# Optimization experiments

Measured on AMD Instinct MI355X. Metric: run time of the kernel, lower is better.

Reference implementation:

```python
import jax, jax.numpy as jnp
import numpy as np
from jax import lax

B, T = 4, 2048
IN_CH, SKIP_CH, OUT_CH, K = 256, 128, 128, 5
N_MAMBA, D_STATE, D_CONV, EXPAND = 2, 16, 4, 2
D_INNER = EXPAND * OUT_CH
DT_RANK = (OUT_CH + 15) // 16  # ceil(d_model/16) = 8
L = 2 * T
EPS = 1e-5


def setup_inputs() -> dict:
    key = jax.random.key(0)
    ks = jax.random.split(key, 16)
    def rn(k, shape, s=0.02):
        return jax.random.normal(k, shape, jnp.float32) * s
    A_init = jnp.broadcast_to(jnp.arange(1, D_STATE + 1, dtype=jnp.float32),
                              (N_MAMBA, 2, D_INNER, D_STATE))
    return {
        'x': rn(ks[0], (B, IN_CH, T), 1.0),
        'skip': rn(ks[1], (B, SKIP_CH, L), 1.0),
        'up_w': rn(ks[2], (IN_CH, IN_CH, K)),       # torch ConvTranspose1d weight (in,out,k)
        'up_b': jnp.zeros((IN_CH,), jnp.float32),
        'fus_w': rn(ks[3], (OUT_CH, IN_CH + SKIP_CH)),  # 1x1 conv
        'fus_b': jnp.zeros((OUT_CH,), jnp.float32),
        'gn_w': jnp.ones((OUT_CH,), jnp.float32),
        'gn_b': jnp.zeros((OUT_CH,), jnp.float32),
        'prelu_a': jnp.array(0.25, jnp.float32),
        'ln_w': jnp.ones((N_MAMBA, OUT_CH), jnp.float32),
        'ln_b': jnp.zeros((N_MAMBA, OUT_CH), jnp.float32),
        'in_w': rn(ks[4], (N_MAMBA, 2, 2 * D_INNER, OUT_CH)),
        'conv_w': rn(ks[5], (N_MAMBA, 2, D_INNER, D_CONV), 0.1),
        'conv_b': jnp.zeros((N_MAMBA, 2, D_INNER), jnp.float32),
        'xproj_w': rn(ks[6], (N_MAMBA, 2, DT_RANK + 2 * D_STATE, D_INNER)),
        'dtproj_w': rn(ks[7], (N_MAMBA, 2, D_INNER, DT_RANK), 0.1),
        'dtproj_b': rn(ks[8], (N_MAMBA, 2, D_INNER), 0.1),
        'A_log': jnp.log(A_init),
        'Dp': jnp.ones((N_MAMBA, 2, D_INNER), jnp.float32),
        'out_w': rn(ks[9], (N_MAMBA, 2, OUT_CH, D_INNER)),
    }


def _mamba_branch(xn, cw, cb, iw, xw, dw, db, Alog, Dp, ow):
    # xn: [B, L, d_model] -> [B, L, d_model]; standard Mamba selective scan.
    xz = jnp.einsum('bld,ed->ble', xn, iw)            # [B,L,2*D_INNER]
    xi, z = jnp.split(xz, 2, axis=-1)
    # causal depthwise conv over time
    xc = lax.conv_general_dilated(xi.transpose(0, 2, 1), cw[:, None, :], (1,),
                                  [(D_CONV - 1, 0)], feature_group_count=D_INNER,
                                  dimension_numbers=('NCH', 'OIH', 'NCH'))
    xi = jax.nn.silu(xc + cb[None, :, None]).transpose(0, 2, 1)  # [B,L,D_INNER]
    dbl = jnp.einsum('bld,ed->ble', xi, xw)           # [B,L,DT_RANK+2N]
    dt = jax.nn.softplus(jnp.einsum('blr,dr->bld', dbl[..., :DT_RANK], dw) + db)
    Bc = dbl[..., DT_RANK:DT_RANK + D_STATE]          # [B,L,N]
    Cc = dbl[..., DT_RANK + D_STATE:]                 # [B,L,N]
    A = -jnp.exp(Alog)                                # [D_INNER,N]
    dA = jnp.exp(dt[..., None] * A)                   # [B,L,D_INNER,N]
    dBx = dt[..., None] * Bc[:, :, None, :] * xi[..., None]
    def comb(c1, c2):
        a1, b1 = c1
        a2, b2 = c2
        return a1 * a2, a2 * b1 + b2
    _, h = lax.associative_scan(comb, (dA, dBx), axis=1)  # h_t = dA_t h_{t-1} + dBx_t
    y = jnp.einsum('bldn,bln->bld', h, Cc) + Dp * xi
    return jnp.einsum('ble,de->bld', y * jax.nn.silu(z), ow)


def _forward(x, skip, up_w, up_b, fus_w, fus_b, gn_w, gn_b, prelu_a, ln_w, ln_b,
             in_w, conv_w, conv_b, xproj_w, dtproj_w, dtproj_b, A_log, Dp, out_w):
    p = K // 2
    # ConvTranspose1d(stride=2, padding=p, output_padding=1) == lhs-dilated conv with flipped kernel
    wt = jnp.flip(up_w, -1).transpose(1, 0, 2)        # (out,in,k)
    u = lax.conv_general_dilated(x, wt, (1,), [(K - 1 - p, K - 1 - p + 1)],
                                 lhs_dilation=(2,),
                                 dimension_numbers=('NCH', 'OIH', 'NCH'))
    u = u + up_b[None, :, None]
    u = u[..., :skip.shape[-1]]
    h = jnp.concatenate([u, skip], axis=1)            # [B, in+skip, L]
    h = jnp.einsum('bct,oc->bot', h, fus_w) + fus_b[None, :, None]
    # GroupNorm(1, C): normalize over (C,T) per sample
    mu = h.mean(axis=(1, 2), keepdims=True)
    var = h.var(axis=(1, 2), keepdims=True)
    h = (h - mu) / jnp.sqrt(var + EPS) * gn_w[None, :, None] + gn_b[None, :, None]
    h = jnp.where(h >= 0, h, prelu_a * h)             # PReLU (single param)
    h = h.transpose(0, 2, 1)                          # [B, L, C]
    for i in range(N_MAMBA):
        # BiMambaBlock: pre-LN, forward + time-reversed Mamba, residual sum
        mu2 = h.mean(-1, keepdims=True)
        v2 = h.var(-1, keepdims=True)
        xn = (h - mu2) / jnp.sqrt(v2 + EPS) * ln_w[i] + ln_b[i]
        f = _mamba_branch(xn, conv_w[i, 0], conv_b[i, 0], in_w[i, 0], xproj_w[i, 0],
                          dtproj_w[i, 0], dtproj_b[i, 0], A_log[i, 0], Dp[i, 0], out_w[i, 0])
        b = _mamba_branch(jnp.flip(xn, 1), conv_w[i, 1], conv_b[i, 1], in_w[i, 1], xproj_w[i, 1],
                          dtproj_w[i, 1], dtproj_b[i, 1], A_log[i, 1], Dp[i, 1], out_w[i, 1])
        h = h + f + jnp.flip(b, 1)
    return h.transpose(0, 2, 1)                       # [B, C_out, L]


def reference(x, skip, up_w, up_b, fus_w, fus_b, gn_w, gn_b, prelu_a, ln_w, ln_b,
              in_w, conv_w, conv_b, xproj_w, dtproj_w, dtproj_b, A_log, Dp, out_w):
    return _forward(x, skip, up_w, up_b, fus_w, fus_b, gn_w, gn_b, prelu_a, ln_w, ln_b,
                    in_w, conv_w, conv_b, xproj_w, dtproj_w, dtproj_b, A_log, Dp, out_w)
```

## Files before the change

kernel.cpp:

```cpp
#include <hip/hip_runtime.h>
#include <hip/hip_bf16.h>

#define Bsz 4
#define Tt 2048
#define Ll 4096
#define NC 256
#define CH 16

typedef short bf16x8 __attribute__((ext_vector_type(8)));
typedef float f32x4 __attribute__((ext_vector_type(4)));
typedef float f32x2 __attribute__((ext_vector_type(2)));

static __device__ __forceinline__ f32x2 pk_fma(f32x2 a, f32x2 b, f32x2 c){
  f32x2 d;
  asm("v_pk_fma_f32 %0, %1, %2, %3" : "=v"(d) : "v"(a), "v"(b), "v"(c));
  return d;
}
static __device__ __forceinline__ f32x2 pk_mul(f32x2 a, f32x2 b){
  f32x2 d;
  asm("v_pk_mul_f32 %0, %1, %2" : "=v"(d) : "v"(a), "v"(b));
  return d;
}
static __device__ __forceinline__ f32x2 lo2(f32x4 v){ return (f32x2){v.x, v.y}; }
static __device__ __forceinline__ f32x2 hi2(f32x4 v){ return (f32x2){v.z, v.w}; }

static __device__ __forceinline__ float bs2f(unsigned short u){
  union{float f; unsigned int i;} v; v.i = ((unsigned int)u)<<16; return v.f;
}
static __device__ __forceinline__ unsigned short f2bs(float f){
  union{float f; unsigned int i;} v; v.f = f;
  unsigned int r = (v.i + 0x7fffu + ((v.i>>16)&1u)) >> 16;
  return (unsigned short)r;
}

__global__ void k_cvt(const float* __restrict__ src, unsigned short* __restrict__ dst, int n){
  int i = blockIdx.x*256 + threadIdx.x;
  if (i < n) dst[i] = f2bs(src[i]);
}

__global__ void k_prepx(const float* __restrict__ xw, unsigned short* __restrict__ wxb){
  int row = blockIdx.x, br = blockIdx.y, col = threadIdx.x;
  float v = (row < 40) ? xw[((size_t)br*40 + row)*256 + col] : 0.f;
  wxb[((size_t)br*64 + row)*256 + col] = f2bs(v);
}

__global__ void k_prepA(const float* __restrict__ Alog, float* __restrict__ AEX,
                        float* __restrict__ A0C, float* __restrict__ CHN){
  int br = blockIdx.x, d = threadIdx.x;
  float A[16];
  #pragma unroll
  for (int j=0;j<4;j++){
    float4 a4 = *(const float4*)&Alog[(size_t)br*4096 + d*16 + j*4];
    A[4*j]  = -__expf(a4.x); A[4*j+1] = -__expf(a4.y);
    A[4*j+2]= -__expf(a4.z); A[4*j+3] = -__expf(a4.w);
    *(float4*)&AEX[(size_t)br*4096 + d*16 + j*4] = (float4){A[4*j],A[4*j+1],A[4*j+2],A[4*j+3]};
  }
  bool chain = true;
  #pragma unroll
  for (int n=1;n<16;n++){
    float expect = A[0]*(float)(n+1);
    if (fabsf(A[n]-expect) > 1e-3f*fabsf(expect)) chain = false;
  }
  A0C[br*256 + d] = A[0];
  CHN[br*256 + d] = chain ? 1.f : 0.f;
}

__global__ void k_compose(const float* __restrict__ up_w, const float* __restrict__ fus_w,
                          const float* __restrict__ fus_b, const float* __restrict__ up_b,
                          unsigned short* __restrict__ WEb, unsigned short* __restrict__ WOb,
                          unsigned short* __restrict__ FWSb, float* __restrict__ BIAS2){
  int i = blockIdx.x;
  int o = threadIdx.x;
  float a0=0.f,a1=0.f,a2=0.f,a3=0.f,a4=0.f;
  for (int c=0;c<256;c++){
    float f = fus_w[o*384+c];
    const float* w = up_w + ((size_t)i*256+c)*5;
    a0 += f*w[0]; a1 += f*w[1]; a2 += f*w[2];
    a3 += f*w[3]; a4 += f*w[4];
  }
  WEb[(size_t)o*768 +       i] = f2bs(a4);
  WEb[(size_t)o*768 + 256 + i] = f2bs(a2);
  WEb[(size_t)o*768 + 512 + i] = f2bs(a0);
  WOb[(size_t)o*512 +       i] = f2bs(a3);
  WOb[(size_t)o*512 + 256 + i] = f2bs(a1);
  if (i<128) FWSb[o*128 + i] = f2bs(fus_w[o*384+256+i]);
  if (i==0){
    float bb = fus_b[o];
    for (int c=0;c<256;c++) bb += fus_w[o*384+c]*up_b[c];
    BIAS2[o]=bb;
  }
// ... 368 lines not shown
  int tid = threadIdx.x;
  int dir = blockIdx.y;
  xz  += (size_t)dir*Bsz*Ll*512;
  wxb += (size_t)dir*64*256;
  cw  += dir*1024;
  cb  += dir*256;
  xib += (size_t)dir*Bsz*Ll*256;
  dbl += (size_t)dir*Bsz*Ll*40;
  size_t row0 = (size_t)blockIdx.x*64;
  int p0 = (int)(row0 & (Ll-1));

  {
    int d = tid;
    float4 w4 = *(const float4*)&cw[d*4];
    float bias = cb[d];
    float w0, w1, w2;
    if (p0 == 0){ w0=0.f; w1=0.f; w2=0.f; }
    else {
      w0 = bs2f(xz[(row0-3)*512 + d]);
      w1 = bs2f(xz[(row0-2)*512 + d]);
      w2 = bs2f(xz[(row0-1)*512 + d]);
    }
    #pragma unroll 4
    for (int rr=0; rr<64; rr++){
      float xv = bs2f(xz[(row0+rr)*512 + d]);
      float acc = bias + w4.x*w0 + w4.y*w1 + w4.z*w2 + w4.w*xv;
      float v = acc*__builtin_amdgcn_rcpf(1.f+__expf(-acc));
      unsigned short us = f2bs(v);
      xiS[rr*264 + d] = us;
      xib[(row0+rr)*256 + d] = us;
      w0=w1; w1=w2; w2=xv;
    }
  }

  int wave = tid>>6, lane = tid&63;
  int quad = lane>>4, l16 = lane&15;
  f32x4 acc[4];
  #pragma unroll
  for (int j=0;j<4;j++) acc[j] = (f32x4){0.f,0.f,0.f,0.f};

  for (int kb=0; kb<256; kb+=64){
    __syncthreads();
    #pragma unroll
    for (int it=0; it<2; it++){
      int idx = it*256 + tid;
      int row = idx>>3, c8 = idx&7;
      *(uint4*)&Bs[row*72 + c8*8] = *(const uint4*)&wxb[(size_t)row*256 + kb + c8*8];
    }
    __syncthreads();
    #pragma unroll
    for (int ks=0; ks<64; ks+=32){
      bf16x8 af = *(bf16x8*)&xiS[(wave*16+l16)*264 + kb + ks + quad*8];
      #pragma unroll
      for (int nt=0;nt<4;nt++){
        bf16x8 bf = *(bf16x8*)&Bs[(nt*16+l16)*72 + ks + quad*8];
        acc[nt] = __builtin_amdgcn_mfma_f32_16x16x32_bf16(af, bf, acc[nt], 0,0,0);
      }
    }
  }
  #pragma unroll
  for (int nt=0;nt<4;nt++)
    #pragma unroll
    for (int r=0;r<4;r++){
      int m = wave*16 + quad*4 + r;
      int col = nt*16 + l16;
      if (col < 40) dbl[(row0+m)*40 + col] = acc[nt][r];
    }
}

#define POWTREE2(e1, pw2) { \
  float _e2 = (e1)*(e1); \
  f32x2 _e2v = (f32x2){_e2,_e2}; \
  pw2[0] = (f32x2){(e1),_e2}; \
  pw2[1] = pk_mul(pw2[0], _e2v); \
  pw2[2] = pk_mul(pw2[1], _e2v); \
  pw2[3] = pk_mul(pw2[2], _e2v); \
  f32x2 _e8v = (f32x2){pw2[3].y, pw2[3].y}; \
  pw2[4] = pk_mul(pw2[0], _e8v); \
  pw2[5] = pk_mul(pw2[1], _e8v); \
  pw2[6] = pk_mul(pw2[2], _e8v); \
  pw2[7] = pk_mul(pw2[3], _e8v); }

__global__ __launch_bounds__(256) void k_scan1(const float* __restrict__ dbl,
                       const unsigned short* __restrict__ xib, const float* __restrict__ AEX,
                       const float* __restrict__ A0C, const float* __restrict__ CHNf,
                       const float* __restrict__ dtw, const float* __restrict__ dtb,
                       float* __restrict__ SD, float* __restrict__ Q){
  __shared__ float dblS[CH*24];
  int b = blockIdx.y, c = blockIdx.x, dir = blockIdx.z;
  int d = threadIdx.x;
  const float* dblP = dbl + (size_t)dir*Bsz*Ll*40;
  const unsigned short* xiP = xib + (size_t)dir*Bsz*Ll*256;
  size_t base = (size_t)b*Ll + (size_t)c*CH;
  if (d < CH*6){
    int p = d/6, j = d - p*6;
    *(float4*)&dblS[p*24 + j*4] = *(const float4*)&dblP[(base+p)*40 + j*4];
  }
  float A0 = A0C[dir*256 + d];
  bool chain = CHNf[dir*256 + d] != 0.f;
  f32x2 wv2[4];
  {
    const float* dw = dtw + (size_t)dir*2048 + d*8;
    float4 w0 = *(const float4*)&dw[0];
    float4 w1 = *(const float4*)&dw[4];
    wv2[0]=(f32x2){w0.x,w0.y}; wv2[1]=(f32x2){w0.z,w0.w};
    wv2[2]=(f32x2){w1.x,w1.y}; wv2[3]=(f32x2){w1.z,w1.w};
  }
  float bbt = dtb[dir*256 + d];
  __syncthreads();
  float sdt = 0.f;
  const unsigned short* xip = xiP + base*256 + d;
  size_t sbase = (size_t)dir*Bsz*NC*4096 + ((size_t)(b*NC + c))*4096 + (size_t)d*16;
  if (chain){
    bool n1 = fabsf(A0 + 1.f) < 1e-6f;
    float xv[CH];
    #pragma unroll
    for (int p=0;p<CH;p++) xv[p] = bs2f(xip[(size_t)p*256]);
    f32x2 h2[8];
    #pragma unroll
    for (int i=0;i<8;i++) h2[i] = (f32x2){0.f,0.f};
    #pragma unroll
    for (int p=0;p<CH;p++){
      const float* rw = &dblS[p*24];
      f32x4 t0 = *(const f32x4*)&rw[0];
      f32x4 t1 = *(const f32x4*)&rw[4];
      f32x2 dp = pk_mul(lo2(t0), wv2[0]);
      dp = pk_fma(hi2(t0), wv2[1], dp);
      dp = pk_fma(lo2(t1), wv2[2], dp);
      dp = pk_fma(hi2(t1), wv2[3], dp);
      float a0 = bbt + dp.x + dp.y;
      float t = __expf(a0);
      float u = 1.f + t;
      float dtv = (a0>20.f)? a0 : __logf(u);
      float e1 = n1 ? __builtin_amdgcn_rcpf(u) : __expf(dtv*A0);
      float dx = dtv*xv[p];
      sdt += dtv;
      f32x2 pw2[8];
      POWTREE2(e1, pw2);
      f32x2 dxv = (f32x2){dx,dx};
      f32x4 b0 = *(const f32x4*)&dblS[p*24+8];
      f32x4 b1 = *(const f32x4*)&dblS[p*24+12];
      f32x4 b2 = *(const f32x4*)&dblS[p*24+16];
      f32x4 b3 = *(const f32x4*)&dblS[p*24+20];
      h2[0] = pk_fma(pw2[0], h2[0], pk_mul(lo2(b0), dxv));
      h2[1] = pk_fma(pw2[1], h2[1], pk_mul(hi2(b0), dxv));
      h2[2] = pk_fma(pw2[2], h2[2], pk_mul(lo2(b1), dxv));
      h2[3] = pk_fma(pw2[3], h2[3], pk_mul(hi2(b1), dxv));
      h2[4] = pk_fma(pw2[4], h2[4], pk_mul(lo2(b2), dxv));
      h2[5] = pk_fma(pw2[5], h2[5], pk_mul(hi2(b2), dxv));
      h2[6] = pk_fma(pw2[6], h2[6], pk_mul(lo2(b3), dxv));
      h2[7] = pk_fma(pw2[7], h2[7], pk_mul(hi2(b3), dxv));
    }
    #pragma unroll
    for (int j=0;j<4;j++)
      *(float4*)&Q[sbase + 4*j] = (float4){h2[2*j].x,h2[2*j].y,h2[2*j+1].x,h2[2*j+1].y};
  } else {
    float A[16];
    #pragma unroll
    for (int j=0;j<4;j++)
      *(float4*)&A[4*j] = *(const float4*)&AEX[(size_t)dir*4096 + d*16 + j*4];
    float h[16];
    #pragma unroll
    for (int n=0;n<16;n++) h[n]=0.f;
    for (int p=0;p<CH;p++){
      const float* rw = &dblS[p*24];
      float4 t0 = *(const float4*)&rw[0], t1 = *(const float4*)&rw[4];
      float a0 = bbt + t0.x*wv2[0].x+t0.y*wv2[0].y+t0.z*wv2[1].x+t0.w*wv2[1].y
                     + t1.x*wv2[2].x+t1.y*wv2[2].y+t1.z*wv2[3].x+t1.w*wv2[3].y;
      float dtv = (a0>20.f)? a0 : __logf(1.f+__expf(a0));
      float xiv = bs2f(xip[(size_t)p*256]);
      float dx = dtv*xiv;
      sdt += dtv;
      float bc[16];
      *(float4*)&bc[0]  = *(const float4*)&rw[8];
      *(float4*)&bc[4]  = *(const float4*)&rw[12];
      *(float4*)&bc[8]  = *(const float4*)&rw[16];
      *(float4*)&bc[12] = *(const float4*)&rw[20];
      #pragma unroll
      for (int n=0;n<16;n++){
        float a = __expf(dtv*A[n]);
        h[n] = a*h[n] + bc[n]*dx;
      }
    }
    #pragma unroll
    for (int j=0;j<4;j++)
      *(float4*)&Q[sbase + 4*j] = (float4){h[4*j],h[4*j+1],h[4*j+2],h[4*j+3]};
  }
  SD[(((size_t)dir*Bsz + b)*NC + c)*256 + d] = sdt;
}

__global__ __launch_bounds__(64) void k_scan2(const float* __restrict__ SD, float* __restrict__ Q,
                                              const float* __restrict__ AEX){
  int b = blockIdx.y, dir = blockIdx.z;
  int t = blockIdx.x*64 + threadIdx.x;
  int dn4 = t*4;
  int d = dn4 >> 4;
  float4 A4 = *(const float4*)&AEX[(size_t)dir*4096 + dn4];
  const float* sd = SD + (((size_t)dir*Bsz + b)*NC)*256 + d;
  float* q = Q + (size_t)dir*Bsz*NC*4096 + (size_t)b*NC*4096 + dn4;
  float4 H = {0.f,0.f,0.f,0.f};
  float  s_n = sd[0];
  float4 q_n = *(const float4*)q;
  for (int c=0;c<NC;c++){
    float s_c = s_n; float4 q_c = q_n;
    if (c+1 < NC){
      s_n = sd[(size_t)(c+1)*256];
      q_n = *(const float4*)(q + (size_t)(c+1)*4096);
    }
    float4 p;
    p.x = __expf(A4.x*s_c); p.y = __expf(A4.y*s_c);
    p.z = __expf(A4.z*s_c); p.w = __expf(A4.w*s_c);
    *(float4*)(q + (size_t)c*4096) = H;
    H.x = p.x*H.x + q_c.x; H.y = p.y*H.y + q_c.y;
    H.z = p.z*H.z + q_c.z; H.w = p.w*H.w + q_c.w;
  }
}

__global__ __launch_bounds__(256) void k_scan3(const float* __restrict__ dbl,
                       unsigned short* xiy, const float* __restrict__ AEX,
                       const float* __restrict__ A0C, const float* __restrict__ CHNf,
                       const float* __restrict__ dtw, const float* __restrict__ dtb,
                       const float* __restrict__ Dpw, const float* __restrict__ Hs,
                       const unsigned short* __restrict__ xz){
  __shared__ float dblS[CH*40];
  int b = blockIdx.y, c = blockIdx.x, dir = blockIdx.z;
  int d = threadIdx.x;
  const float* dblP = dbl + (size_t)dir*Bsz*Ll*40;
  unsigned short* xiP = xiy + (size_t)dir*Bsz*Ll*256;
  const unsigned short* xzP = xz + (size_t)dir*Bsz*Ll*512;
  size_t base = (size_t)b*Ll + (size_t)c*CH;
  for (int idx=d; idx<CH*10; idx+=256){
    int p = idx/10, j = idx - p*10;
    *(float4*)&dblS[p*40 + j*4] = *(const float4*)&dblP[(base+p)*40 + j*4];
  }
  float A0 = A0C[dir*256 + d];
  bool chain = CHNf[dir*256 + d] != 0.f;
  f32x2 wv2[4];
  {
    const float* dw = dtw + (size_t)dir*2048 + d*8;
    float4 w0 = *(const float4*)&dw[0];
    float4 w1 = *(const float4*)&dw[4];
    wv2[0]=(f32x2){w0.x,w0.y}; wv2[1]=(f32x2){w0.z,w0.w};
    wv2[2]=(f32x2){w1.x,w1.y}; wv2[3]=(f32x2){w1.z,w1.w};
  }
  float bbt = dtb[dir*256 + d];
  float Dp = Dpw[dir*256 + d];
  size_t sbase = (size_t)dir*Bsz*NC*4096 + ((size_t)(b*NC + c))*4096 + (size_t)d*16;
  __syncthreads();
  unsigned short* xip = xiP + base*256 + d;
  const unsigned short* zp = xzP + base*512 + 256 + d;
  if (chain){
    bool n1 = fabsf(A0 + 1.f) < 1e-6f;
    float xv[CH], zv[CH];
    #pragma unroll
    for (int p=0;p<CH;p++) xv[p] = bs2f(xip[(size_t)p*256]);
    #pragma unroll
    for (int p=0;p<CH;p++) zv[p] = bs2f(zp[(size_t)p*512]);
    f32x2 h2[8];
    #pragma unroll
    for (int j=0;j<4;j++){
      float4 h4 = *(const float4*)&Hs[sbase + 4*j];
      h2[2*j]   = (f32x2){h4.x,h4.y};
      h2[2*j+1] = (f32x2){h4.z,h4.w};
    }
    #pragma unroll
    for (int p=0;p<CH;p++){
      const float* rw = &dblS[p*40];
      f32x4 t0 = *(const f32x4*)&rw[0];
      f32x4 t1 = *(const f32x4*)&rw[4];
      f32x2 dp = pk_mul(lo2(t0), wv2[0]);
      dp = pk_fma(hi2(t0), wv2[1], dp);
      dp = pk_fma(lo2(t1), wv2[2], dp);
      dp = pk_fma(hi2(t1), wv2[3], dp);
      float a0 = bbt + dp.x + dp.y;
      float t = __expf(a0);
      float u = 1.f + t;
      float dtv = (a0>20.f)? a0 : __logf(u);
      float e1 = n1 ? __builtin_amdgcn_rcpf(u) : __expf(dtv*A0);
      float dx = dtv*xv[p];
      f32x2 pw2[8];
      POWTREE2(e1, pw2);
      f32x2 dxv = (f32x2){dx,dx};
      f32x4 b0 = *(const f32x4*)&dblS[p*40+8];
      f32x4 b1 = *(const f32x4*)&dblS[p*40+12];
      f32x4 b2 = *(const f32x4*)&dblS[p*40+16];
      f32x4 b3 = *(const f32x4*)&dblS[p*40+20];
      f32x4 c0 = *(const f32x4*)&dblS[p*40+24];
      f32x4 c1 = *(const f32x4*)&dblS[p*40+28];
      f32x4 c2 = *(const f32x4*)&dblS[p*40+32];
      f32x4 c3 = *(const f32x4*)&dblS[p*40+36];
      f32x2 ya;
      h2[0] = pk_fma(pw2[0], h2[0], pk_mul(lo2(b0), dxv));
      ya = pk_mul(h2[0], lo2(c0));
      h2[1] = pk_fma(pw2[1], h2[1], pk_mul(hi2(b0), dxv));
      ya = pk_fma(h2[1], hi2(c0), ya);
      h2[2] = pk_fma(pw2[2], h2[2], pk_mul(lo2(b1), dxv));
      ya = pk_fma(h2[2], lo2(c1), ya);
      h2[3] = pk_fma(pw2[3], h2[3], pk_mul(hi2(b1), dxv));
      ya = pk_fma(h2[3], hi2(c1), ya);
      h2[4] = pk_fma(pw2[4], h2[4], pk_mul(lo2(b2), dxv));
      ya = pk_fma(h2[4], lo2(c2), ya);
      h2[5] = pk_fma(pw2[5], h2[5], pk_mul(hi2(b2), dxv));
      ya = pk_fma(h2[5], hi2(c2), ya);
      h2[6] = pk_fma(pw2[6], h2[6], pk_mul(lo2(b3), dxv));
      ya = pk_fma(h2[6], lo2(c3), ya);
      h2[7] = pk_fma(pw2[7], h2[7], pk_mul(hi2(b3), dxv));
      ya = pk_fma(h2[7], hi2(c3), ya);
      float acc = ya.x + ya.y;
      float z = zv[p];
      float g = z*__builtin_amdgcn_rcpf(1.f+__expf(-z));
      xip[(size_t)p*256] = f2bs((acc + Dp*xv[p])*g);
    }
  } else {
    float A[16];
    #pragma unroll
    for (int j=0;j<4;j++)
      *(float4*)&A[4*j] = *(const float4*)&AEX[(size_t)dir*4096 + d*16 + j*4];
    float h[16];
    #pragma unroll
    for (int j=0;j<4;j++){
      float4 h4 = *(const float4*)&Hs[sbase + 4*j];
      h[4*j]=h4.x; h[4*j+1]=h4.y; h[4*j+2]=h4.z; h[4*j+3]=h4.w;
    }
    for (int p=0;p<CH;p++){
      const float* rw = &dblS[p*40];
      float4 t0 = *(const float4*)&rw[0], t1 = *(const float4*)&rw[4];
      float a0 = bbt + t0.x*wv2[0].x+t0.y*wv2[0].y+t0.z*wv2[1].x+t0.w*wv2[1].y
                     + t1.x*wv2[2].x+t1.y*wv2[2].y+t1.z*wv2[3].x+t1.w*wv2[3].y;
      float dtv = (a0>20.f)? a0 : __logf(1.f+__expf(a0));
      float xiv = bs2f(xip[(size_t)p*256]);
      float dx = dtv*xiv;
      float bc[16], cc[16];
      *(float4*)&bc[0]  = *(const float4*)&rw[8];
      *(float4*)&bc[4]  = *(const float4*)&rw[12];
      *(float4*)&bc[8]  = *(const float4*)&rw[16];
      *(float4*)&bc[12] = *(const float4*)&rw[20];
      *(float4*)&cc[0]  = *(const float4*)&rw[24];
      *(float4*)&cc[4]  = *(const float4*)&rw[28];
      *(float4*)&cc[8]  = *(const float4*)&rw[32];
      *(float4*)&cc[12] = *(const float4*)&rw[36];
      float acc = 0.f;
      #pragma unroll
      for (int n=0;n<16;n++){
        float a = __expf(dtv*A[n]);
        h[n] = a*h[n] + bc[n]*dx;
        acc += h[n]*cc[n];
      }
      float z = bs2f(zp[(size_t)p*512]);
      float g = z*__builtin_amdgcn_rcpf(1.f+__expf(-z));
      xip[(size_t)p*256] = f2bs((acc + Dp*xiv)*g);
    }
  }
}

__global__ __launch_bounds__(256) void k_final(const float* __restrict__ hres, float* __restrict__ out){
  __shared__ float tile[64*129];
  int b = blockIdx.y, l0 = blockIdx.x*64;
  int tid = threadIdx.x;
  for (int q=0;q<32;q++){
    int idx = q*256 + tid;
    int l = idx >> 7, c = idx & 127;
    tile[l*129 + c] = hres[((size_t)b*Ll + l0 + l)*128 + c];
  }
  __syncthreads();
  int lo = tid & 63; int cbase = tid >> 6;
  for (int q=0;q<32;q++){
    int c = cbase + q*4;
    out[((size_t)b*128 + c)*Ll + l0 + lo] = tile[lo*129 + c];
  }
}

extern "C" void kernel_launch(void* const* d_in, const int* in_sizes, int n_in,
                              void* d_out, int out_size, void* d_ws, size_t ws_size,
                              hipStream_t stream){
  const float* x      = (const float*)d_in[0];
  const float* skip   = (const float*)d_in[1];
  const float* up_w   = (const float*)d_in[2];
  const float* up_b   = (const float*)d_in[3];
  const float* fus_w  = (const float*)d_in[4];
  const float* fus_b  = (const float*)d_in[5];
  const float* gn_w   = (const float*)d_in[6];
  const float* gn_b   = (const float*)d_in[7];
  const float* pa     = (const float*)d_in[8];
  const float* ln_w   = (const float*)d_in[9];
  const float* ln_b   = (const float*)d_in[10];
  const float* in_w   = (const float*)d_in[11];
  const float* conv_w = (const float*)d_in[12];
  const float* conv_b = (const float*)d_in[13];
  const float* xproj_w= (const float*)d_in[14];
  const float* dtproj_w=(const float*)d_in[15];
  const float* dtproj_b=(const float*)d_in[16];
  const float* A_log  = (const float*)d_in[17];
  const float* Dp     = (const float*)d_in[18];
  const float* out_w  = (const float*)d_in[19];

  float* w = (float*)d_ws;
  size_t off=0;
  float* B2 = w+off; off += 128;
  float* GST= w+off; off += 16;
  off = (off+3)&~(size_t)3;
  float* HR = w+off; off += (size_t)Bsz*Ll*128;
  float* DBL2= w+off; off += 2*(size_t)Bsz*Ll*40;
  unsigned short* XNB = (unsigned short*)(w+off); off += (size_t)Bsz*Ll*128/2;
  unsigned short* XZB2= (unsigned short*)(w+off); off += 2*(size_t)Bsz*Ll*512/2;
  unsigned short* IWB = (unsigned short*)(w+off); off += 2*2*512*128/2;
  unsigned short* OWB = (unsigned short*)(w+off); off += 2*2*128*256/2;
  unsigned short* WXB = (unsigned short*)(w+off); off += 2*2*64*256/2;
  unsigned short* WEb = (unsigned short*)(w+off); off += 768*128/2;
  unsigned short* WOb = (unsigned short*)(w+off); off += 512*128/2;
  unsigned short* FWSb= (unsigned short*)(w+off); off += 128*128/2;
  float* AEXb = w+off; off += 4*4096;
  float* A0Cb = w+off; off += 4*256;
  float* CHNb = w+off; off += 4*256;
  size_t planeS = (size_t)Bsz*NC*4096;
  float* U1 = w+off; off += 2*planeS;
  unsigned short* XT  = (unsigned short*)U1;
  unsigned short* SKT = (unsigned short*)(U1 + 1049604);
  float* SQ = U1;
  float* SD = (float*)XNB;
  float* U2 = w+off; off += 2*(size_t)Bsz*Ll*128;
  float* H0 = U2;
  unsigned short* XIB2 = (unsigned short*)U2;

  hipMemsetAsync(GST, 0, 16*sizeof(float), stream);
  k_cvt<<<(2*2*512*128+255)/256,256,0,stream>>>(in_w, IWB, 2*2*512*128);
  k_cvt<<<(2*2*128*256+255)/256,256,0,stream>>>(out_w, OWB, 2*2*128*256);
  k_prepx<<<dim3(64,4),256,0,stream>>>(xproj_w, WXB);
  k_prepA<<<4,256,0,stream>>>(A_log, AEXb, A0Cb, CHNb);
  k_compose<<<256,128,0,stream>>>(up_w, fus_w, fus_b, up_b, WEb, WOb, FWSb, B2);
  k_tx<<<dim3(Tt/64, 4, Bsz),256,0,stream>>>(x, XT);
  k_zero<<<1,256,0,stream>>>(XT);
  k_ts<<<dim3(Ll/64, 2, Bsz),256,0,stream>>>(skip, SKT);
  k_up<<<dim3(32, 2, Bsz),256,0,stream>>>(XT, SKT, WEb, WOb, FWSb, B2, H0, GST);
  k_gnfin<<<1,64,0,stream>>>(GST);
  k_gnln<<<Bsz*Ll/4,256,0,stream>>>(H0, gn_w, gn_b, pa, GST, ln_w, ln_b, HR, XNB);
  for (int i=0;i<2;i++){
    k_gemm_in<<<dim3(128,4,2),256,0,stream>>>(XNB, IWB + (size_t)(i*2)*512*128, XZB2);
    k_xproj3<<<dim3(Bsz*Ll/64,2),256,0,stream>>>(XZB2, WXB + (size_t)(i*2)*64*256,
                                                 conv_w + (i*2)*1024, conv_b + (i*2)*256,
                                                 XIB2, DBL2);
    k_scan1<<<dim3(NC,Bsz,2),256,0,stream>>>(DBL2, XIB2, AEXb + (size_t)(i*2)*4096,
                                             A0Cb + (i*2)*256, CHNb + (i*2)*256,
                                             dtproj_w + (i*2)*2048, dtproj_b + (i*2)*256, SD, SQ);
    k_scan2<<<dim3(16,Bsz,2),64,0,stream>>>(SD, SQ, AEXb + (size_t)(i*2)*4096);
    k_scan3<<<dim3(NC,Bsz,2),256,0,stream>>>(DBL2, XIB2, AEXb + (size_t)(i*2)*4096,
                                             A0Cb + (i*2)*256, CHNb + (i*2)*256,
                                             dtproj_w + (i*2)*2048, dtproj_b + (i*2)*256,
                                             Dp + (i*2)*256, SQ, XZB2);
    if (i==0)
      k_gemm_out_t<1><<<256,256,0,stream>>>(XIB2, OWB + 0, HR, ln_w + 128, ln_b + 128, XNB);
    else
      k_gemm_out_t<0><<<256,256,0,stream>>>(XIB2, OWB + (size_t)2*128*256, HR,
                                            (const float*)nullptr, (const float*)nullptr,
                                            (unsigned short*)nullptr);
  }
  k_final<<<dim3(Ll/64,Bsz),256,0,stream>>>(HR, (float*)d_out);
}
```

Measured before the change: 412.4 us.

## Move intra-chunk scan output into pass one, make pass three a carry correction

The first scan pass now computes each chunk's local output (C·h plus the D skip term) from a zero initial state and writes it over the xi buffer. The third pass then only adds the carried-in state's contribution, using a running product of per-step decays and C·H, instead of redoing the full state recurrence. This takes the B·dx update and its dependency chain out of the third pass, at the cost of more shared-memory loads and global stores in the first pass. The inter-chunk scan kernel also prefetches two chunks ahead instead of one.

```diff
diff --git a/kernel.cpp b/kernel.cpp
--- a/kernel.cpp
+++ b/kernel.cpp
@@ -540,19 +540,20 @@
   pw2[7] = pk_mul(pw2[3], _e8v); }
 
 __global__ __launch_bounds__(256) void k_scan1(const float* __restrict__ dbl,
-                       const unsigned short* __restrict__ xib, const float* __restrict__ AEX,
+                       unsigned short* __restrict__ xib, const float* __restrict__ AEX,
                        const float* __restrict__ A0C, const float* __restrict__ CHNf,
                        const float* __restrict__ dtw, const float* __restrict__ dtb,
+                       const float* __restrict__ Dpw,
                        float* __restrict__ SD, float* __restrict__ Q){
-  __shared__ float dblS[CH*24];
+  __shared__ float dblS[CH*40];
   int b = blockIdx.y, c = blockIdx.x, dir = blockIdx.z;
   int d = threadIdx.x;
   const float* dblP = dbl + (size_t)dir*Bsz*Ll*40;
-  const unsigned short* xiP = xib + (size_t)dir*Bsz*Ll*256;
+  unsigned short* xiP = xib + (size_t)dir*Bsz*Ll*256;
   size_t base = (size_t)b*Ll + (size_t)c*CH;
-  if (d < CH*6){
-    int p = d/6, j = d - p*6;
-    *(float4*)&dblS[p*24 + j*4] = *(const float4*)&dblP[(base+p)*40 + j*4];
+  for (int idx=d; idx<CH*10; idx+=256){
+    int p = idx/10, j = idx - p*10;
+    *(float4*)&dblS[p*40 + j*4] = *(const float4*)&dblP[(base+p)*40 + j*4];
   }
   float A0 = A0C[dir*256 + d];
   bool chain = CHNf[dir*256 + d] != 0.f;
@@ -565,9 +566,10 @@
     wv2[2]=(f32x2){w1.x,w1.y}; wv2[3]=(f32x2){w1.z,w1.w};
   }
   float bbt = dtb[dir*256 + d];
+  float Dp = Dpw[dir*256 + d];
   __syncthreads();
   float sdt = 0.f;
-  const unsigned short* xip = xiP + base*256 + d;
+  unsigned short* xip = xiP + base*256 + d;
   size_t sbase = (size_t)dir*Bsz*NC*4096 + ((size_t)(b*NC + c))*4096 + (size_t)d*16;
   if (chain){
     bool n1 = fabsf(A0 + 1.f) < 1e-6f;
@@ -577,150 +579,6 @@
     f32x2 h2[8];
     #pragma unroll
     for (int i=0;i<8;i++) h2[i] = (f32x2){0.f,0.f};
-    #pragma unroll
-    for (int p=0;p<CH;p++){
-      const float* rw = &dblS[p*24];
-      f32x4 t0 = *(const f32x4*)&rw[0];
-      f32x4 t1 = *(const f32x4*)&rw[4];
-      f32x2 dp = pk_mul(lo2(t0), wv2[0]);
-      dp = pk_fma(hi2(t0), wv2[1], dp);
-      dp = pk_fma(lo2(t1), wv2[2], dp);
-      dp = pk_fma(hi2(t1), wv2[3], dp);
-      float a0 = bbt + dp.x + dp.y;
-      float t = __expf(a0);
-      float u = 1.f + t;
-      float dtv = (a0>20.f)? a0 : __logf(u);
-      float e1 = n1 ? __builtin_amdgcn_rcpf(u) : __expf(dtv*A0);
-      float dx = dtv*xv[p];
-      sdt += dtv;
-      f32x2 pw2[8];
-      POWTREE2(e1, pw2);
-      f32x2 dxv = (f32x2){dx,dx};
-      f32x4 b0 = *(const f32x4*)&dblS[p*24+8];
-      f32x4 b1 = *(const f32x4*)&dblS[p*24+12];
-      f32x4 b2 = *(const f32x4*)&dblS[p*24+16];
-      f32x4 b3 = *(const f32x4*)&dblS[p*24+20];
-      h2[0] = pk_fma(pw2[0], h2[0], pk_mul(lo2(b0), dxv));
-      h2[1] = pk_fma(pw2[1], h2[1], pk_mul(hi2(b0), dxv));
-      h2[2] = pk_fma(pw2[2], h2[2], pk_mul(lo2(b1), dxv));
-      h2[3] = pk_fma(pw2[3], h2[3], pk_mul(hi2(b1), dxv));
-      h2[4] = pk_fma(pw2[4], h2[4], pk_mul(lo2(b2), dxv));
-      h2[5] = pk_fma(pw2[5], h2[5], pk_mul(hi2(b2), dxv));
-      h2[6] = pk_fma(pw2[6], h2[6], pk_mul(lo2(b3), dxv));
-      h2[7] = pk_fma(pw2[7], h2[7], pk_mul(hi2(b3), dxv));
-    }
-    #pragma unroll
-    for (int j=0;j<4;j++)
-      *(float4*)&Q[sbase + 4*j] = (float4){h2[2*j].x,h2[2*j].y,h2[2*j+1].x,h2[2*j+1].y};
-  } else {
-    float A[16];
-    #pragma unroll
-    for (int j=0;j<4;j++)
-      *(float4*)&A[4*j] = *(const float4*)&AEX[(size_t)dir*4096 + d*16 + j*4];
-    float h[16];
-    #pragma unroll
-    for (int n=0;n<16;n++) h[n]=0.f;
-    for (int p=0;p<CH;p++){
-      const float* rw = &dblS[p*24];
-      float4 t0 = *(const float4*)&rw[0], t1 = *(const float4*)&rw[4];
-      float a0 = bbt + t0.x*wv2[0].x+t0.y*wv2[0].y+t0.z*wv2[1].x+t0.w*wv2[1].y
-                     + t1.x*wv2[2].x+t1.y*wv2[2].y+t1.z*wv2[3].x+t1.w*wv2[3].y;
-      float dtv = (a0>20.f)? a0 : __logf(1.f+__expf(a0));
-      float xiv = bs2f(xip[(size_t)p*256]);
-      float dx = dtv*xiv;
-      sdt += dtv;
-      float bc[16];
-      *(float4*)&bc[0]  = *(const float4*)&rw[8];
-      *(float4*)&bc[4]  = *(const float4*)&rw[12];
-      *(float4*)&bc[8]  = *(const float4*)&rw[16];
-      *(float4*)&bc[12] = *(const float4*)&rw[20];
-      #pragma unroll
-      for (int n=0;n<16;n++){
-        float a = __expf(dtv*A[n]);
-        h[n] = a*h[n] + bc[n]*dx;
-      }
-    }
-    #pragma unroll
-    for (int j=0;j<4;j++)
-      *(float4*)&Q[sbase + 4*j] = (float4){h[4*j],h[4*j+1],h[4*j+2],h[4*j+3]};
-  }
-  SD[(((size_t)dir*Bsz + b)*NC + c)*256 + d] = sdt;
-}
-
-__global__ __launch_bounds__(64) void k_scan2(const float* __restrict__ SD, float* __restrict__ Q,
-                                              const float* __restrict__ AEX){
-  int b = blockIdx.y, dir = blockIdx.z;
-  int t = blockIdx.x*64 + threadIdx.x;
-  int dn4 = t*4;
-  int d = dn4 >> 4;
-  float4 A4 = *(const float4*)&AEX[(size_t)dir*4096 + dn4];
-  const float* sd = SD + (((size_t)dir*Bsz + b)*NC)*256 + d;
-  float* q = Q + (size_t)dir*Bsz*NC*4096 + (size_t)b*NC*4096 + dn4;
-  float4 H = {0.f,0.f,0.f,0.f};
-  float  s_n = sd[0];
-  float4 q_n = *(const float4*)q;
-  for (int c=0;c<NC;c++){
-    float s_c = s_n; float4 q_c = q_n;
-    if (c+1 < NC){
-      s_n = sd[(size_t)(c+1)*256];
-      q_n = *(const float4*)(q + (size_t)(c+1)*4096);
-    }
-    float4 p;
-    p.x = __expf(A4.x*s_c); p.y = __expf(A4.y*s_c);
-    p.z = __expf(A4.z*s_c); p.w = __expf(A4.w*s_c);
-    *(float4*)(q + (size_t)c*4096) = H;
-    H.x = p.x*H.x + q_c.x; H.y = p.y*H.y + q_c.y;
-    H.z = p.z*H.z + q_c.z; H.w = p.w*H.w + q_c.w;
-  }
-}
-
-__global__ __launch_bounds__(256) void k_scan3(const float* __restrict__ dbl,
-                       unsigned short* xiy, const float* __restrict__ AEX,
-                       const float* __restrict__ A0C, const float* __restrict__ CHNf,
-                       const float* __restrict__ dtw, const float* __restrict__ dtb,
-                       const float* __restrict__ Dpw, const float* __restrict__ Hs,
-                       const unsigned short* __restrict__ xz){
-  __shared__ float dblS[CH*40];
-  int b = blockIdx.y, c = blockIdx.x, dir = blockIdx.z;
-  int d = threadIdx.x;
-  const float* dblP = dbl + (size_t)dir*Bsz*Ll*40;
-  unsigned short* xiP = xiy + (size_t)dir*Bsz*Ll*256;
-  const unsigned short* xzP = xz + (size_t)dir*Bsz*Ll*512;
-  size_t base = (size_t)b*Ll + (size_t)c*CH;
-  for (int idx=d; idx<CH*10; idx+=256){
-    int p = idx/10, j = idx - p*10;
-    *(float4*)&dblS[p*40 + j*4] = *(const float4*)&dblP[(base+p)*40 + j*4];
-  }
-  float A0 = A0C[dir*256 + d];
-  bool chain = CHNf[dir*256 + d] != 0.f;
-  f32x2 wv2[4];
-  {
-    const float* dw = dtw + (size_t)dir*2048 + d*8;
-    float4 w0 = *(const float4*)&dw[0];
-    float4 w1 = *(const float4*)&dw[4];
-    wv2[0]=(f32x2){w0.x,w0.y}; wv2[1]=(f32x2){w0.z,w0.w};
-    wv2[2]=(f32x2){w1.x,w1.y}; wv2[3]=(f32x2){w1.z,w1.w};
-  }
-  float bbt = dtb[dir*256 + d];
-  float Dp = Dpw[dir*256 + d];
-  size_t sbase = (size_t)dir*Bsz*NC*4096 + ((size_t)(b*NC + c))*4096 + (size_t)d*16;
-  __syncthreads();
-  unsigned short* xip = xiP + base*256 + d;
-  const unsigned short* zp = xzP + base*512 + 256 + d;
-  if (chain){
-    bool n1 = fabsf(A0 + 1.f) < 1e-6f;
-    float xv[CH], zv[CH];
-    #pragma unroll
-    for (int p=0;p<CH;p++) xv[p] = bs2f(xip[(size_t)p*256]);
-    #pragma unroll
-    for (int p=0;p<CH;p++) zv[p] = bs2f(zp[(size_t)p*512]);
-    f32x2 h2[8];
-    #pragma unroll
-    for (int j=0;j<4;j++){
-      float4 h4 = *(const float4*)&Hs[sbase + 4*j];
-      h2[2*j]   = (f32x2){h4.x,h4.y};
-      h2[2*j+1] = (f32x2){h4.z,h4.w};
-    }
     #pragma unroll
     for (int p=0;p<CH;p++){
       const float* rw = &dblS[p*40];
@@ -736,6 +594,7 @@
       float dtv = (a0>20.f)? a0 : __logf(u);
       float e1 = n1 ? __builtin_amdgcn_rcpf(u) : __expf(dtv*A0);
       float dx = dtv*xv[p];
+      sdt += dtv;
       f32x2 pw2[8];
       POWTREE2(e1, pw2);
       f32x2 dxv = (f32x2){dx,dx};
@@ -764,10 +623,159 @@
       ya = pk_fma(h2[6], lo2(c3), ya);
       h2[7] = pk_fma(pw2[7], h2[7], pk_mul(hi2(b3), dxv));
       ya = pk_fma(h2[7], hi2(c3), ya);
-      float acc = ya.x + ya.y;
+      float ylb = ya.x + ya.y + Dp*xv[p];
+      xip[(size_t)p*256] = f2bs(ylb);
+    }
+    #pragma unroll
+    for (int j=0;j<4;j++)
+      *(float4*)&Q[sbase + 4*j] = (float4){h2[2*j].x,h2[2*j].y,h2[2*j+1].x,h2[2*j+1].y};
+  } else {
+    float A[16];
+    #pragma unroll
+    for (int j=0;j<4;j++)
+      *(float4*)&A[4*j] = *(const float4*)&AEX[(size_t)dir*4096 + d*16 + j*4];
+    float h[16];
+    #pragma unroll
+    for (int n=0;n<16;n++) h[n]=0.f;
+    for (int p=0;p<CH;p++){
+      const float* rw = &dblS[p*40];
+      float4 t0 = *(const float4*)&rw[0], t1 = *(const float4*)&rw[4];
+      float a0 = bbt + t0.x*wv2[0].x+t0.y*wv2[0].y+t0.z*wv2[1].x+t0.w*wv2[1].y
+                     + t1.x*wv2[2].x+t1.y*wv2[2].y+t1.z*wv2[3].x+t1.w*wv2[3].y;
+      float dtv = (a0>20.f)? a0 : __logf(1.f+__expf(a0));
+      float xiv = bs2f(xip[(size_t)p*256]);
+      float dx = dtv*xiv;
+      sdt += dtv;
+      float bc[16];
+      *(float4*)&bc[0]  = *(const float4*)&rw[8];
+      *(float4*)&bc[4]  = *(const float4*)&rw[12];
+      *(float4*)&bc[8]  = *(const float4*)&rw[16];
+      *(float4*)&bc[12] = *(const float4*)&rw[20];
+      #pragma unroll
+      for (int n=0;n<16;n++){
+        float a = __expf(dtv*A[n]);
+        h[n] = a*h[n] + bc[n]*dx;
+      }
+    }
+    #pragma unroll
+    for (int j=0;j<4;j++)
+      *(float4*)&Q[sbase + 4*j] = (float4){h[4*j],h[4*j+1],h[4*j+2],h[4*j+3]};
+  }
+  SD[(((size_t)dir*Bsz + b)*NC + c)*256 + d] = sdt;
+}
+
+__global__ __launch_bounds__(64) void k_scan2(const float* __restrict__ SD, float* __restrict__ Q,
+                                              const float* __restrict__ AEX){
+  int b = blockIdx.y, dir = blockIdx.z;
+  int t = blockIdx.x*64 + threadIdx.x;
+  int dn4 = t*4;
+  int d = dn4 >> 4;
+  float4 A4 = *(const float4*)&AEX[(size_t)dir*4096 + dn4];
+  const float* sd = SD + (((size_t)dir*Bsz + b)*NC)*256 + d;
+  float* q = Q + (size_t)dir*Bsz*NC*4096 + (size_t)b*NC*4096 + dn4;
+  float4 H = {0.f,0.f,0.f,0.f};
+  float  s_a = sd[0];
+  float4 q_a = *(const float4*)q;
+  float  s_b = sd[256];
+  float4 q_b = *(const float4*)(q + 4096);
+  for (int c=0;c<NC;c++){
+    float s_c = s_a; float4 q_c = q_a;
+    s_a = s_b; q_a = q_b;
+    if (c+2 < NC){
+      s_b = sd[(size_t)(c+2)*256];
+      q_b = *(const float4*)(q + (size_t)(c+2)*4096);
+    }
+    float4 p;
+    p.x = __expf(A4.x*s_c); p.y = __expf(A4.y*s_c);
+    p.z = __expf(A4.z*s_c); p.w = __expf(A4.w*s_c);
+    *(float4*)(q + (size_t)c*4096) = H;
+    H.x = p.x*H.x + q_c.x; H.y = p.y*H.y + q_c.y;
+    H.z = p.z*H.z + q_c.z; H.w = p.w*H.w + q_c.w;
+  }
+}
+
+__global__ __launch_bounds__(256) void k_scan3(const float* __restrict__ dbl,
+                       unsigned short* xiy, const float* __restrict__ AEX,
+                       const float* __restrict__ A0C, const float* __restrict__ CHNf,
+                       const float* __restrict__ dtw, const float* __restrict__ dtb,
+                       const float* __restrict__ Dpw, const float* __restrict__ Hs,
+                       const unsigned short* __restrict__ xz){
+  __shared__ float dblS[CH*40];
+  int b = blockIdx.y, c = blockIdx.x, dir = blockIdx.z;
+  int d = threadIdx.x;
+  const float* dblP = dbl + (size_t)dir*Bsz*Ll*40;
+  unsigned short* xiP = xiy + (size_t)dir*Bsz*Ll*256;
+  const unsigned short* xzP = xz + (size_t)dir*Bsz*Ll*512;
+  size_t base = (size_t)b*Ll + (size_t)c*CH;
+  for (int idx=d; idx<CH*10; idx+=256){
+    int p = idx/10, j = idx - p*10;
+    *(float4*)&dblS[p*40 + j*4] = *(const float4*)&dblP[(base+p)*40 + j*4];
+  }
+  float A0 = A0C[dir*256 + d];
+  bool chain = CHNf[dir*256 + d] != 0.f;
+  f32x2 wv2[4];
+  {
+    const float* dw = dtw + (size_t)dir*2048 + d*8;
+    float4 w0 = *(const float4*)&dw[0];
+    float4 w1 = *(const float4*)&dw[4];
+    wv2[0]=(f32x2){w0.x,w0.y}; wv2[1]=(f32x2){w0.z,w0.w};
+    wv2[2]=(f32x2){w1.x,w1.y}; wv2[3]=(f32x2){w1.z,w1.w};
+  }
+  float bbt = dtb[dir*256 + d];
+  float Dp = Dpw[dir*256 + d];
+  size_t sbase = (size_t)dir*Bsz*NC*4096 + ((size_t)(b*NC + c))*4096 + (size_t)d*16;
+  __syncthreads();
+  unsigned short* xip = xiP + base*256 + d;
+  const unsigned short* zp = xzP + base*512 + 256 + d;
+  if (chain){
+    bool n1 = fabsf(A0 + 1.f) < 1e-6f;
+    float yv[CH], zv[CH];
+    #pragma unroll
+    for (int p=0;p<CH;p++) yv[p] = bs2f(xip[(size_t)p*256]);
+    #pragma unroll
+    for (int p=0;p<CH;p++) zv[p] = bs2f(zp[(size_t)p*512]);
+    f32x2 Hv[8];
+    #pragma unroll
+    for (int j=0;j<4;j++){
+      float4 h4 = *(const float4*)&Hs[sbase + 4*j];
+      Hv[2*j]   = (f32x2){h4.x,h4.y};
+      Hv[2*j+1] = (f32x2){h4.z,h4.w};
+    }
+    float ecum = 1.f;
+    #pragma unroll
+    for (int p=0;p<CH;p++){
+      const float* rw = &dblS[p*40];
+      f32x4 t0 = *(const f32x4*)&rw[0];
+      f32x4 t1 = *(const f32x4*)&rw[4];
+      f32x2 dp = pk_mul(lo2(t0), wv2[0]);
+      dp = pk_fma(hi2(t0), wv2[1], dp);
+      dp = pk_fma(lo2(t1), wv2[2], dp);
+      dp = pk_fma(hi2(t1), wv2[3], dp);
+      float a0 = bbt + dp.x + dp.y;
+      float t = __expf(a0);
+      float u = 1.f + t;
+      float dtv = (a0>20.f)? a0 : __logf(u);
+      float e1 = n1 ? __builtin_amdgcn_rcpf(u) : __expf(dtv*A0);
+      ecum *= e1;
+      f32x2 pw2[8];
+      POWTREE2(ecum, pw2);
+      f32x4 c0 = *(const f32x4*)&dblS[p*40+24];
+      f32x4 c1 = *(const f32x4*)&dblS[p*40+28];
+      f32x4 c2 = *(const f32x4*)&dblS[p*40+32];
+      f32x4 c3 = *(const f32x4*)&dblS[p*40+36];
+      f32x2 ya;
+      ya = pk_mul(pw2[0], pk_mul(lo2(c0), Hv[0]));
+      ya = pk_fma(pw2[1], pk_mul(hi2(c0), Hv[1]), ya);
+      ya = pk_fma(pw2[2], pk_mul(lo2(c1), Hv[2]), ya);
+      ya = pk_fma(pw2[3], pk_mul(hi2(c1), Hv[3]), ya);
+      ya = pk_fma(pw2[4], pk_mul(lo2(c2), Hv[4]), ya);
+      ya = pk_fma(pw2[5], pk_mul(hi2(c2), Hv[5]), ya);
+      ya = pk_fma(pw2[6], pk_mul(lo2(c3), Hv[6]), ya);
+      ya = pk_fma(pw2[7], pk_mul(hi2(c3), Hv[7]), ya);
+      float y = yv[p] + ya.x + ya.y;
       float z = zv[p];
       float g = z*__builtin_amdgcn_rcpf(1.f+__expf(-z));
-      xip[(size_t)p*256] = f2bs((acc + Dp*xv[p])*g);
+      xip[(size_t)p*256] = f2bs(y*g);
     }
   } else {
     float A[16];
@@ -899,7 +907,8 @@
                                                  XIB2, DBL2);
     k_scan1<<<dim3(NC,Bsz,2),256,0,stream>>>(DBL2, XIB2, AEXb + (size_t)(i*2)*4096,
                                              A0Cb + (i*2)*256, CHNb + (i*2)*256,
-                                             dtproj_w + (i*2)*2048, dtproj_b + (i*2)*256, SD, SQ);
+                                             dtproj_w + (i*2)*2048, dtproj_b + (i*2)*256,
+                                             Dp + (i*2)*256, SD, SQ);
     k_scan2<<<dim3(16,Bsz,2),64,0,stream>>>(SD, SQ, AEXb + (size_t)(i*2)*4096);
     k_scan3<<<dim3(NC,Bsz,2),256,0,stream>>>(DBL2, XIB2, AEXb + (size_t)(i*2)*4096,
                                              A0Cb + (i*2)*256, CHNb + (i*2)*256,
```

After: 452.5 us. +9.7%, slower.

## Split sequential chunk-state scan into two-level hierarchical scan

Applied to the files above, without the earlier changes.

The single serial pass over 256 chunks in k_scan2, which ran only 128 blocks of 64 threads, is replaced by a two-level scan. First, 16 groups per sequence each scan their own chunks locally and write group totals. Second, a short serial scan runs over the 16 group totals. k_scan3 then folds the group carry into each chunk's starting state using exp(A*prefix dt). This exposes more parallelism in the latency-bound carry scan, at the cost of an extra kernel launch and extra exponentials and loads in k_scan3.

```diff
diff --git a/kernel.cpp b/kernel.cpp
--- a/kernel.cpp
+++ b/kernel.cpp
@@ -6,6 +6,7 @@
 #define Ll 4096
 #define NC 256
 #define CH 16
+#define NG 16
 
 typedef short bf16x8 __attribute__((ext_vector_type(8)));
 typedef float f32x4 __attribute__((ext_vector_type(4)));
@@ -647,30 +648,58 @@
   SD[(((size_t)dir*Bsz + b)*NC + c)*256 + d] = sdt;
 }
 
-__global__ __launch_bounds__(64) void k_scan2(const float* __restrict__ SD, float* __restrict__ Q,
-                                              const float* __restrict__ AEX){
+__global__ __launch_bounds__(64) void k_scan2a(float* __restrict__ SD, float* __restrict__ Q,
+                        float* __restrict__ SDG, float* __restrict__ QG,
+                        const float* __restrict__ AEX){
+  int zb = blockIdx.z;
+  int dir = zb >> 2;
+  int g  = blockIdx.y;
+  int t  = blockIdx.x*64 + threadIdx.x;
+  int dn4 = t*4;
+  int d = dn4 >> 4;
+  float4 A4 = *(const float4*)&AEX[(size_t)dir*4096 + dn4];
+  float* sd = SD + (((size_t)zb*NC) + (size_t)g*(NC/NG))*256 + d;
+  float* q  = Q + (size_t)zb*NC*4096 + (size_t)g*(NC/NG)*4096 + dn4;
+  float4 H = {0.f,0.f,0.f,0.f};
+  float S = 0.f;
+  #pragma unroll
+  for (int c2=0; c2<NC/NG; c2++){
+    float s_c = sd[(size_t)c2*256];
+    float4 q_c = *(const float4*)(q + (size_t)c2*4096);
+    sd[(size_t)c2*256] = S;
+    *(float4*)(q + (size_t)c2*4096) = H;
+    float4 p;
+    p.x = __expf(A4.x*s_c); p.y = __expf(A4.y*s_c);
+    p.z = __expf(A4.z*s_c); p.w = __expf(A4.w*s_c);
+    H.x = p.x*H.x + q_c.x; H.y = p.y*H.y + q_c.y;
+    H.z = p.z*H.z + q_c.z; H.w = p.w*H.w + q_c.w;
+    S += s_c;
+  }
+  SDG[((size_t)zb*NG + g)*256 + d] = S;
+  *(float4*)&QG[((size_t)zb*NG + g)*4096 + dn4] = H;
+}
+
+__global__ __launch_bounds__(64) void k_scan2b(const float* __restrict__ SDG, float* __restrict__ QG,
+                        const float* __restrict__ AEX){
   int b = blockIdx.y, dir = blockIdx.z;
+  int zb = dir*Bsz + b;
   int t = blockIdx.x*64 + threadIdx.x;
   int dn4 = t*4;
   int d = dn4 >> 4;
   float4 A4 = *(const float4*)&AEX[(size_t)dir*4096 + dn4];
-  const float* sd = SD + (((size_t)dir*Bsz + b)*NC)*256 + d;
-  float* q = Q + (size_t)dir*Bsz*NC*4096 + (size_t)b*NC*4096 + dn4;
+  const float* sg = SDG + (size_t)zb*NG*256 + d;
+  float* qg = QG + (size_t)zb*NG*4096 + dn4;
   float4 H = {0.f,0.f,0.f,0.f};
-  float  s_n = sd[0];
-  float4 q_n = *(const float4*)q;
-  for (int c=0;c<NC;c++){
-    float s_c = s_n; float4 q_c = q_n;
-    if (c+1 < NC){
-      s_n = sd[(size_t)(c+1)*256];
-      q_n = *(const float4*)(q + (size_t)(c+1)*4096);
-    }
+  #pragma unroll
+  for (int g=0; g<NG; g++){
+    float s = sg[(size_t)g*256];
+    float4 qe = *(const float4*)(qg + (size_t)g*4096);
+    *(float4*)(qg + (size_t)g*4096) = H;
     float4 p;
-    p.x = __expf(A4.x*s_c); p.y = __expf(A4.y*s_c);
-    p.z = __expf(A4.z*s_c); p.w = __expf(A4.w*s_c);
-    *(float4*)(q + (size_t)c*4096) = H;
-    H.x = p.x*H.x + q_c.x; H.y = p.y*H.y + q_c.y;
-    H.z = p.z*H.z + q_c.z; H.w = p.w*H.w + q_c.w;
+    p.x = __expf(A4.x*s); p.y = __expf(A4.y*s);
+    p.z = __expf(A4.z*s); p.w = __expf(A4.w*s);
+    H.x = p.x*H.x + qe.x; H.y = p.y*H.y + qe.y;
+    H.z = p.z*H.z + qe.z; H.w = p.w*H.w + qe.w;
   }
 }
 
@@ -679,6 +708,7 @@
                        const float* __restrict__ A0C, const float* __restrict__ CHNf,
                        const float* __restrict__ dtw, const float* __restrict__ dtb,
                        const float* __restrict__ Dpw, const float* __restrict__ Hs,
+                       const float* __restrict__ SDp, const float* __restrict__ QG,
                        const unsigned short* __restrict__ xz){
   __shared__ float dblS[CH*40];
   int b = blockIdx.y, c = blockIdx.x, dir = blockIdx.z;
@@ -703,7 +733,10 @@
   }
   float bbt = dtb[dir*256 + d];
   float Dp = Dpw[dir*256 + d];
-  size_t sbase = (size_t)dir*Bsz*NC*4096 + ((size_t)(b*NC + c))*4096 + (size_t)d*16;
+  int zb = dir*Bsz + b;
+  size_t sbase = (size_t)zb*NC*4096 + (size_t)c*4096 + (size_t)d*16;
+  float sdtp = SDp[(((size_t)zb)*NC + c)*256 + d];
+  size_t gbase = ((size_t)zb*NG + (c >> 4))*4096 + (size_t)d*16;
   __syncthreads();
   unsigned short* xip = xiP + base*256 + d;
   const unsigned short* zp = xzP + base*512 + 256 + d;
@@ -715,11 +748,17 @@
     #pragma unroll
     for (int p=0;p<CH;p++) zv[p] = bs2f(zp[(size_t)p*512]);
     f32x2 h2[8];
-    #pragma unroll
-    for (int j=0;j<4;j++){
-      float4 h4 = *(const float4*)&Hs[sbase + 4*j];
-      h2[2*j]   = (f32x2){h4.x,h4.y};
-      h2[2*j+1] = (f32x2){h4.z,h4.w};
+    {
+      float eg = __expf(A0*sdtp);
+      f32x2 pg[8];
+      POWTREE2(eg, pg);
+      #pragma unroll
+      for (int j=0;j<4;j++){
+        float4 h4 = *(const float4*)&Hs[sbase + 4*j];
+        float4 g4 = *(const float4*)&QG[gbase + 4*j];
+        h2[2*j]   = pk_fma(pg[2*j],   (f32x2){g4.x,g4.y}, (f32x2){h4.x,h4.y});
+        h2[2*j+1] = pk_fma(pg[2*j+1], (f32x2){g4.z,g4.w}, (f32x2){h4.z,h4.w});
+      }
     }
     #pragma unroll
     for (int p=0;p<CH;p++){
@@ -778,7 +817,11 @@
     #pragma unroll
     for (int j=0;j<4;j++){
       float4 h4 = *(const float4*)&Hs[sbase + 4*j];
-      h[4*j]=h4.x; h[4*j+1]=h4.y; h[4*j+2]=h4.z; h[4*j+3]=h4.w;
+      float4 g4 = *(const float4*)&QG[gbase + 4*j];
+      h[4*j]   = __expf(A[4*j]*sdtp)*g4.x   + h4.x;
+      h[4*j+1] = __expf(A[4*j+1]*sdtp)*g4.y + h4.y;
+      h[4*j+2] = __expf(A[4*j+2]*sdtp)*g4.z + h4.z;
+      h[4*j+3] = __expf(A[4*j+3]*sdtp)*g4.w + h4.w;
     }
     for (int p=0;p<CH;p++){
       const float* rw = &dblS[p*40];
@@ -870,12 +913,14 @@
   float* AEXb = w+off; off += 4*4096;
   float* A0Cb = w+off; off += 4*256;
   float* CHNb = w+off; off += 4*256;
+  float* SDGb = w+off; off += (size_t)2*Bsz*NG*256;
   size_t planeS = (size_t)Bsz*NC*4096;
   float* U1 = w+off; off += 2*planeS;
   unsigned short* XT  = (unsigned short*)U1;
   unsigned short* SKT = (unsigned short*)(U1 + 1049604);
   float* SQ = U1;
   float* SD = (float*)XNB;
+  float* QG = SD + 524288;
   float* U2 = w+off; off += 2*(size_t)Bsz*Ll*128;
   float* H0 = U2;
   unsigned short* XIB2 = (unsigned short*)U2;
@@ -900,11 +945,12 @@
     k_scan1<<<dim3(NC,Bsz,2),256,0,stream>>>(DBL2, XIB2, AEXb + (size_t)(i*2)*4096,
                                              A0Cb + (i*2)*256, CHNb + (i*2)*256,
                                              dtproj_w + (i*2)*2048, dtproj_b + (i*2)*256, SD, SQ);
-    k_scan2<<<dim3(16,Bsz,2),64,0,stream>>>(SD, SQ, AEXb + (size_t)(i*2)*4096);
+    k_scan2a<<<dim3(16,NG,2*Bsz),64,0,stream>>>(SD, SQ, SDGb, QG, AEXb + (size_t)(i*2)*4096);
+    k_scan2b<<<dim3(16,Bsz,2),64,0,stream>>>(SDGb, QG, AEXb + (size_t)(i*2)*4096);
     k_scan3<<<dim3(NC,Bsz,2),256,0,stream>>>(DBL2, XIB2, AEXb + (size_t)(i*2)*4096,
                                              A0Cb + (i*2)*256, CHNb + (i*2)*256,
                                              dtproj_w + (i*2)*2048, dtproj_b + (i*2)*256,
-                                             Dp + (i*2)*256, SQ, XZB2);
+                                             Dp + (i*2)*256, SQ, SD, QG, XZB2);
     if (i==0)
       k_gemm_out_t<1><<<256,256,0,stream>>>(XIB2, OWB + 0, HR, ln_w + 128, ln_b + 128, XNB);
     else
```

After: 393.9 us. 4.5% less time.
